# Kernel optimization log

Measured on AMD Instinct MI355X. Metric: run time of the kernel, lower is better.

Reference implementation:

```python
import jax, jax.numpy as jnp
import numpy as np

K = 3  # reassembly kernel size (hardcoded in module)
S = 2  # upsample scale (hardcoded)
PAD = K // 2


def _nearest_up2(t):
    # F.interpolate(scale_factor=2, mode='nearest') on NCHW
    return jnp.repeat(jnp.repeat(t, 2, axis=2), 2, axis=3)


def _patches3x3(t):
    # F.unfold(kernel=3, pad=1) -> [B, C, 9, H, W], k = ki*3 + kj (row-major)
    B, C, H, W = t.shape
    tp = jnp.pad(t, ((0, 0), (0, 0), (PAD, PAD), (PAD, PAD)))
    return jnp.stack([tp[:, :, i:i + H, j:j + W] for i in range(K) for j in range(K)], axis=2)


def setup_inputs() -> dict:
    key = jax.random.key(0)
    k1, k2 = jax.random.split(key)
    x = jax.random.normal(k1, (2, 256, 128, 128), dtype=jnp.float32)
    W_off = jax.random.normal(k2, (2, 1, 5, 5), dtype=jnp.float32) * 1e-3  # normal_init std=0.001
    b_off = jnp.zeros((2,), dtype=jnp.float32)
    return {"x": x, "W_off": W_off, "b_off": b_off}


def reference(x, W_off, b_off):
    B, C, H, W = x.shape
    H2, W2 = S * H, S * W

    mean = jnp.mean(x, axis=1, keepdims=True)  # [B,1,H,W]

    # offset = tanh(conv5x5(nearest_up2(mean))) / 4 -> [B,2,2H,2W]
    mean_up = _nearest_up2(mean)
    off = jax.lax.conv_general_dilated(mean_up, W_off, (1, 1), ((2, 2), (2, 2)))
    offset = jnp.tanh(off + b_off[None, :, None, None]) / 4.0

    # center buffer: pixel_shuffle of [1,8,1,1]; per 2x2 cell, channel 0 varies with j, channel 1 with i
    cell = jnp.array([[[-0.25, 0.25], [-0.25, 0.25]],
                      [[-0.25, -0.25], [0.25, 0.25]]], dtype=x.dtype)  # [2(ch),2(i),2(j)]
    center = jnp.broadcast_to(cell[:, None, :, None, :], (2, H, 2, W, 2)).reshape(2, H2, W2)

    shift = center[None] + offset  # [B,2,2H,2W]

    # neighbor grid: n0 (fast, width) = [-1,0,1]*3 ; n1 (slow, height) = repeat([-1,0,1],3)
    n0 = jnp.tile(jnp.array([-1.0, 0.0, 1.0], dtype=x.dtype), 3)        # [9]
    n1 = jnp.repeat(jnp.array([-1.0, 0.0, 1.0], dtype=x.dtype), 3)      # [9]
    d2 = (shift[:, 0:1] - n0[None, :, None, None]) ** 2 + \
         (shift[:, 1:2] - n1[None, :, None, None]) ** 2                 # [B,9,2H,2W]
    kernels = 1.0 / (d2 + 0.2)

    # grad gating from 3x3 neighborhood of mean
    pm = _patches3x3(mean)[:, 0]            # [B,9,H,W]
    grad = pm - mean                        # broadcast over k
    grad = 1.0 / (grad ** 2 + 1.0)
    logits = _nearest_up2(grad) * kernels   # [B,9,2H,2W]
    kernels = jax.nn.softmax(logits, axis=1)

    # CARAFE: out[b,c,2h+p,2w+q] = sum_k kernels[b,k,2h+p,2w+q] * patches[b,c,k,h,w]
    patches = _patches3x3(x)                        # [B,C,9,H,W]
    Kr = kernels.reshape(B, K * K, H, S, W, S)      # [B,9,H,2,W,2]
    out = jnp.einsum('bkhpwq,bckhw->bchpwq', Kr, patches).reshape(B, C, H2, W2)
    return out
```

## Files before the change

kernel.cpp:

```cpp
#include <hip/hip_runtime.h>
#include <math.h>

#define B 2
#define C 256
#define H 128
#define W 128
#define H2 256
#define W2 256
#define CPT 16
#define TW 16

typedef float vfloat4 __attribute__((ext_vector_type(4)));

__device__ __forceinline__ float frcp(float x) { return __builtin_amdgcn_rcpf(x); }
__device__ __forceinline__ float fast_tanh(float x) {
    float e = __expf(2.0f * x);
    return 1.0f - 2.0f * frcp(e + 1.0f);
}

__device__ __forceinline__ void nt_store4(float* p, const float4& v) {
    vfloat4 t; t.x = v.x; t.y = v.y; t.z = v.z; t.w = v.w;
    __builtin_nontemporal_store(t, (vfloat4*)p);
}

__global__ __launch_bounds__(1024) void mean_kernel(const float* __restrict__ x,
                                                    float* __restrict__ mean) {
    int bh = blockIdx.x;
    int b = bh / H, h = bh % H;
    int tid = threadIdx.x;
    int g  = tid >> 5;
    int w4 = tid & 31;

    const float4* xb = (const float4*)x + (size_t)b * C * (H * W / 4)
                       + (size_t)h * (W / 4) + w4;
    const size_t cstride = H * W / 4;

    float4 acc = make_float4(0.f, 0.f, 0.f, 0.f);
    #pragma unroll
    for (int i = 0; i < C / 32; ++i) {
        float4 v = xb[(size_t)(g * (C / 32) + i) * cstride];
        acc.x += v.x; acc.y += v.y; acc.z += v.z; acc.w += v.w;
    }

    __shared__ float4 sm[1024];
    sm[tid] = acc;
    __syncthreads();
    for (int s = 16; s >= 1; s >>= 1) {
        if (g < s) {
            float4 o = sm[tid + s * 32];
            acc.x += o.x; acc.y += o.y; acc.z += o.z; acc.w += o.w;
            sm[tid] = acc;
        }
        __syncthreads();
    }
    if (g == 0) {
        const float inv = 1.0f / C;
        float4 m = make_float4(acc.x * inv, acc.y * inv, acc.z * inv, acc.w * inv);
        ((float4*)mean)[(size_t)bh * (W / 4) + w4] = m;
    }
}

__global__ __launch_bounds__(256) void weights_kernel(const float* __restrict__ mean,
                                                      const float* __restrict__ Woff,
                                                      const float* __restrict__ boff,
                                                      float* __restrict__ Kw) {
    __shared__ float sm[10][12];
    __shared__ float sW[50];
    __shared__ float sb[2];

    int b  = blockIdx.z;
    int x0 = blockIdx.x * TW;
    int y0 = blockIdx.y * TW;
    int h0 = y0 >> 1, w0 = x0 >> 1;
    int tid = threadIdx.x;

    if (tid < 100) {
        int lh = tid / 10, lw = tid % 10;
        int hh = h0 - 1 + lh, ww = w0 - 1 + lw;
        sm[lh][lw] = (hh >= 0 && hh < H && ww >= 0 && ww < W)
                         ? mean[(size_t)b * H * W + hh * W + ww] : 0.f;
    }
    if (tid >= 128 && tid < 178) sW[tid - 128] = Woff[tid - 128];
    if (tid >= 192 && tid < 194) sb[tid - 192] = boff[tid - 192];
    __syncthreads();

    int tx = tid & 15, ty = tid >> 4;
    int y = y0 + ty, x = x0 + tx;

    float off0 = 0.f, off1 = 0.f;
    #pragma unroll
    for (int u = 0; u < 5; ++u) {
        int lh = ((y + u - 2) >> 1) - (h0 - 1);
        #pragma unroll
        for (int v = 0; v < 5; ++v) {
            int lw = ((x + v - 2) >> 1) - (w0 - 1);
            float m = sm[lh][lw];
            off0 += m * sW[u * 5 + v];
            off1 += m * sW[25 + u * 5 + v];
        }
    }
    float s0 = fast_tanh(off0 + sb[0]) * 0.25f + ((x & 1) ? 0.25f : -0.25f);
    float s1 = fast_tanh(off1 + sb[1]) * 0.25f + ((y & 1) ? 0.25f : -0.25f);

    int lhc = (ty >> 1) + 1;
    int lwc = (tx >> 1) + 1;
    float mc = sm[lhc][lwc];

    float lg[9];
    float mx = -1e30f;
    #pragma unroll
    for (int k = 0; k < 9; ++k) {
        int di = k / 3 - 1, dj = k % 3 - 1;
        float pm = sm[lhc + di][lwc + dj];
        float g = pm - mc;
        float grad = frcp(g * g + 1.0f);
        float d0 = s0 - (float)dj;
        float d1 = s1 - (float)di;
        float kern = frcp(d0 * d0 + d1 * d1 + 0.2f);
        float l = grad * kern;
        lg[k] = l;
        mx = fmaxf(mx, l);
    }
    float sum = 0.f;
    #pragma unroll
    for (int k = 0; k < 9; ++k) { lg[k] = __expf(lg[k] - mx); sum += lg[k]; }
    float inv = frcp(sum);

    float* o = Kw + (size_t)b * 9 * (H2 * W2) + (size_t)y * W2 + x;
    #pragma unroll
    for (int k = 0; k < 9; ++k) o[(size_t)k * (H2 * W2)] = lg[k] * inv;
}

__global__ __launch_bounds__(256) void carafe_kernel(const float* __restrict__ x,
                                                     const float* __restrict__ Kw,
                                                     float* __restrict__ out) {
    int idx = blockIdx.x * blockDim.x + threadIdx.x;
    int w2 = idx & 63;
    int h  = (idx >> 6) & (H - 1);
    int cg = (idx >> 13) & (C / CPT - 1);
    int b  = idx >> 17;

    int x0 = 4 * w2;
    int y0 = 2 * h;

    const float* kb = Kw + (size_t)b * 9 * (H2 * W2) + (size_t)y0 * W2 + x0;
    float4 wk[2][9];
    #pragma unroll
    for (int k = 0; k < 9; ++k) {
        wk[0][k] = *(const float4*)(kb + (size_t)k * (H2 * W2));
        wk[1][k] = *(const float4*)(kb + (size_t)k * (H2 * W2) + W2);
    }

    float rm0 = (h == 0)     ? 0.f : 1.f;
    float rm2 = (h == H - 1) ? 0.f : 1.f;
    float cl  = (w2 == 0)    ? 0.f : 1.f;
    float cr  = (w2 == 63)   ? 0.f : 1.f;
    #pragma unroll
    for (int pp = 0; pp < 2; ++pp)
        #pragma unroll
        for (int k = 0; k < 9; ++k) {
            int ki = k / 3, kj = k % 3;
            float r  = (ki == 0) ? rm0 : ((ki == 2) ? rm2 : 1.f);
            float ma = (kj == 0) ? r * cl : r;
            float mb = (kj == 2) ? r * cr : r;
            wk[pp][k].x *= ma; wk[pp][k].y *= ma;
            wk[pp][k].z *= mb; wk[pp][k].w *= mb;
        }

    int r0 = (h == 0) ? 0 : h - 1;
    int r2 = (h == H - 1) ? H - 1 : h + 1;

    const float* xc = x + (size_t)(b * C + cg * CPT) * (H * W);
    const float2* row0 = (const float2*)(xc + (size_t)r0 * W) + w2;
    const float2* row1 = (const float2*)(xc + (size_t)h  * W) + w2;
    const float2* row2 = (const float2*)(xc + (size_t)r2 * W) + w2;

    float* ob = out + (size_t)(b * C + cg * CPT) * (H2 * W2)
                    + (size_t)y0 * W2 + x0;

    #pragma unroll 2
    for (int cc = 0; cc < CPT; ++cc) {
        float2 v0 = row0[0];
        float2 v1 = row1[0];
        float2 v2 = row2[0];

        float e[3][4];
        e[0][1] = v0.x; e[0][2] = v0.y;
        e[1][1] = v1.x; e[1][2] = v1.y;
        e[2][1] = v2.x; e[2][2] = v2.y;
        e[0][0] = __shfl_up(v0.y, 1);   e[0][3] = __shfl_down(v0.x, 1);
        e[1][0] = __shfl_up(v1.y, 1);   e[1][3] = __shfl_down(v1.x, 1);
        e[2][0] = __shfl_up(v2.y, 1);   e[2][3] = __shfl_down(v2.x, 1);

        float4 a0 = make_float4(0.f, 0.f, 0.f, 0.f);
        float4 a1 = make_float4(0.f, 0.f, 0.f, 0.f);
        #pragma unroll
        for (int k = 0; k < 9; ++k) {
            int ki = k / 3, kj = k % 3;
            float pa = e[ki][kj];
            float pb = e[ki][kj + 1];
            a0.x += wk[0][k].x * pa; a0.y += wk[0][k].y * pa;
            a0.z += wk[0][k].z * pb; a0.w += wk[0][k].w * pb;
            a1.x += wk[1][k].x * pa; a1.y += wk[1][k].y * pa;
            a1.z += wk[1][k].z * pb; a1.w += wk[1][k].w * pb;
        }
        nt_store4(ob, a0);
        nt_store4(ob + W2, a1);

        row0 = (const float2*)((const float*)row0 + H * W);
        row1 = (const float2*)((const float*)row1 + H * W);
        row2 = (const float2*)((const float*)row2 + H * W);
        ob += (size_t)H2 * W2;
    }
}

extern "C" void kernel_launch(void* const* d_in, const int* in_sizes, int n_in,
                              void* d_out, int out_size, void* d_ws, size_t ws_size,
                              hipStream_t stream) {
    const float* x    = (const float*)d_in[0];
    const float* Woff = (const float*)d_in[1];
    const float* boff = (const float*)d_in[2];
    float* out = (float*)d_out;

    float* mean = (float*)d_ws;
    float* Kw   = mean + (size_t)B * H * W;

    mean_kernel<<<B * H, 1024, 0, stream>>>(x, mean);

    dim3 wgrid(W2 / TW, H2 / TW, B);
    weights_kernel<<<wgrid, 256, 0, stream>>>(mean, Woff, boff, Kw);

    int mt = B * (C / CPT) * H * (W / 2);
    carafe_kernel<<<mt / 256, 256, 0, stream>>>(x, Kw, out);
}
```

Baseline: 173.7 us.

## Fuse reassembly-weight computation into CARAFE kernel and drop weight buffer

The separate weights kernel and the 9-plane weight buffer in global memory are removed. Each CARAFE thread now loads its 3x3 neighbourhood of the channel mean, shares edges with its lane neighbours via shuffles, and computes the offset conv, tanh, gating and softmax for its 2x4 output pixels in registers. This removes one launch and the write and re-read of the weight planes. In exchange the weight math is recomputed once per channel group (16 times), which raises ALU work and register pressure. The softmax also drops the max subtraction, relying on the logits being bounded.

```diff
diff --git a/kernel.cpp b/kernel.cpp
--- a/kernel.cpp
+++ b/kernel.cpp
@@ -8,7 +8,6 @@
 #define H2 256
 #define W2 256
 #define CPT 16
-#define TW 16
 
 typedef float vfloat4 __attribute__((ext_vector_type(4)));
 
@@ -17,7 +16,6 @@
     float e = __expf(2.0f * x);
     return 1.0f - 2.0f * frcp(e + 1.0f);
 }
-
 __device__ __forceinline__ void nt_store4(float* p, const float4& v) {
     vfloat4 t; t.x = v.x; t.y = v.y; t.z = v.z; t.w = v.w;
     __builtin_nontemporal_store(t, (vfloat4*)p);
@@ -60,115 +58,97 @@
     }
 }
 
-__global__ __launch_bounds__(256) void weights_kernel(const float* __restrict__ mean,
-                                                      const float* __restrict__ Woff,
-                                                      const float* __restrict__ boff,
-                                                      float* __restrict__ Kw) {
-    __shared__ float sm[10][12];
+__global__ __launch_bounds__(256) void carafe_fused(const float* __restrict__ x,
+                                                    const float* __restrict__ mean,
+                                                    const float* __restrict__ Woff,
+                                                    const float* __restrict__ boff,
+                                                    float* __restrict__ out) {
     __shared__ float sW[50];
     __shared__ float sb[2];
-
-    int b  = blockIdx.z;
-    int x0 = blockIdx.x * TW;
-    int y0 = blockIdx.y * TW;
-    int h0 = y0 >> 1, w0 = x0 >> 1;
     int tid = threadIdx.x;
-
-    if (tid < 100) {
-        int lh = tid / 10, lw = tid % 10;
-        int hh = h0 - 1 + lh, ww = w0 - 1 + lw;
-        sm[lh][lw] = (hh >= 0 && hh < H && ww >= 0 && ww < W)
-                         ? mean[(size_t)b * H * W + hh * W + ww] : 0.f;
-    }
-    if (tid >= 128 && tid < 178) sW[tid - 128] = Woff[tid - 128];
-    if (tid >= 192 && tid < 194) sb[tid - 192] = boff[tid - 192];
+    if (tid < 50) sW[tid] = Woff[tid];
+    else if (tid < 52) sb[tid - 50] = boff[tid - 50];
     __syncthreads();
 
-    int tx = tid & 15, ty = tid >> 4;
-    int y = y0 + ty, x = x0 + tx;
-
-    float off0 = 0.f, off1 = 0.f;
-    #pragma unroll
-    for (int u = 0; u < 5; ++u) {
-        int lh = ((y + u - 2) >> 1) - (h0 - 1);
-        #pragma unroll
-        for (int v = 0; v < 5; ++v) {
-            int lw = ((x + v - 2) >> 1) - (w0 - 1);
-            float m = sm[lh][lw];
-            off0 += m * sW[u * 5 + v];
-            off1 += m * sW[25 + u * 5 + v];
-        }
-    }
-    float s0 = fast_tanh(off0 + sb[0]) * 0.25f + ((x & 1) ? 0.25f : -0.25f);
-    float s1 = fast_tanh(off1 + sb[1]) * 0.25f + ((y & 1) ? 0.25f : -0.25f);
-
-    int lhc = (ty >> 1) + 1;
-    int lwc = (tx >> 1) + 1;
-    float mc = sm[lhc][lwc];
-
-    float lg[9];
-    float mx = -1e30f;
-    #pragma unroll
-    for (int k = 0; k < 9; ++k) {
-        int di = k / 3 - 1, dj = k % 3 - 1;
-        float pm = sm[lhc + di][lwc + dj];
-        float g = pm - mc;
-        float grad = frcp(g * g + 1.0f);
-        float d0 = s0 - (float)dj;
-        float d1 = s1 - (float)di;
-        float kern = frcp(d0 * d0 + d1 * d1 + 0.2f);
-        float l = grad * kern;
-        lg[k] = l;
-        mx = fmaxf(mx, l);
-    }
-    float sum = 0.f;
-    #pragma unroll
-    for (int k = 0; k < 9; ++k) { lg[k] = __expf(lg[k] - mx); sum += lg[k]; }
-    float inv = frcp(sum);
-
-    float* o = Kw + (size_t)b * 9 * (H2 * W2) + (size_t)y * W2 + x;
-    #pragma unroll
-    for (int k = 0; k < 9; ++k) o[(size_t)k * (H2 * W2)] = lg[k] * inv;
-}
-
-__global__ __launch_bounds__(256) void carafe_kernel(const float* __restrict__ x,
-                                                     const float* __restrict__ Kw,
-                                                     float* __restrict__ out) {
-    int idx = blockIdx.x * blockDim.x + threadIdx.x;
+    int idx = blockIdx.x * blockDim.x + tid;
     int w2 = idx & 63;
     int h  = (idx >> 6) & (H - 1);
     int cg = (idx >> 13) & (C / CPT - 1);
     int b  = idx >> 17;
 
-    int x0 = 4 * w2;
-    int y0 = 2 * h;
-
-    const float* kb = Kw + (size_t)b * 9 * (H2 * W2) + (size_t)y0 * W2 + x0;
-    float4 wk[2][9];
-    #pragma unroll
-    for (int k = 0; k < 9; ++k) {
-        wk[0][k] = *(const float4*)(kb + (size_t)k * (H2 * W2));
-        wk[1][k] = *(const float4*)(kb + (size_t)k * (H2 * W2) + W2);
-    }
-
-    float rm0 = (h == 0)     ? 0.f : 1.f;
-    float rm2 = (h == H - 1) ? 0.f : 1.f;
-    float cl  = (w2 == 0)    ? 0.f : 1.f;
-    float cr  = (w2 == 63)   ? 0.f : 1.f;
-    #pragma unroll
-    for (int pp = 0; pp < 2; ++pp)
-        #pragma unroll
-        for (int k = 0; k < 9; ++k) {
-            int ki = k / 3, kj = k % 3;
-            float r  = (ki == 0) ? rm0 : ((ki == 2) ? rm2 : 1.f);
-            float ma = (kj == 0) ? r * cl : r;
-            float mb = (kj == 2) ? r * cr : r;
-            wk[pp][k].x *= ma; wk[pp][k].y *= ma;
-            wk[pp][k].z *= mb; wk[pp][k].w *= mb;
-        }
-
     int r0 = (h == 0) ? 0 : h - 1;
     int r2 = (h == H - 1) ? H - 1 : h + 1;
+    float rm0 = (h == 0)      ? 0.f : 1.f;
+    float rm2 = (h == H - 1)  ? 0.f : 1.f;
+    float cl  = (w2 == 0)     ? 0.f : 1.f;
+    float cr  = (w2 == 63)    ? 0.f : 1.f;
+
+    const float* mb = mean + (size_t)b * H * W;
+    float2 u0 = ((const float2*)(mb + (size_t)r0 * W))[w2];
+    float2 u1 = ((const float2*)(mb + (size_t)h  * W))[w2];
+    float2 u2 = ((const float2*)(mb + (size_t)r2 * W))[w2];
+
+    float m[3][4];
+    m[0][1] = u0.x; m[0][2] = u0.y;
+    m[1][1] = u1.x; m[1][2] = u1.y;
+    m[2][1] = u2.x; m[2][2] = u2.y;
+    m[0][0] = __shfl_up(u0.y, 1);  m[0][3] = __shfl_down(u0.x, 1);
+    m[1][0] = __shfl_up(u1.y, 1);  m[1][3] = __shfl_down(u1.x, 1);
+    m[2][0] = __shfl_up(u2.y, 1);  m[2][3] = __shfl_down(u2.x, 1);
+    #pragma unroll
+    for (int c = 0; c < 4; ++c) { m[0][c] *= rm0; m[2][c] *= rm2; }
+    #pragma unroll
+    for (int r = 0; r < 3; ++r) { m[r][0] *= cl; m[r][3] *= cr; }
+
+    float wgt[2][9][4];
+    #pragma unroll
+    for (int pp = 0; pp < 2; ++pp) {
+        #pragma unroll
+        for (int j = 0; j < 4; ++j) {
+            float off0 = 0.f, off1 = 0.f;
+            #pragma unroll
+            for (int u = 0; u < 5; ++u) {
+                const int rr = ((pp + u - 2) >> 1) + 1;
+                #pragma unroll
+                for (int v = 0; v < 5; ++v) {
+                    const int cc = ((j + v - 2) >> 1) + 1;
+                    float mm = m[rr][cc];
+                    off0 += mm * sW[u * 5 + v];
+                    off1 += mm * sW[25 + u * 5 + v];
+                }
+            }
+            float s0 = fast_tanh(off0 + sb[0]) * 0.25f + ((j & 1) ? 0.25f : -0.25f);
+            float s1 = fast_tanh(off1 + sb[1]) * 0.25f + (pp ? 0.25f : -0.25f);
+
+            const int jc = 1 + (j >> 1);
+            float mc = m[1][jc];
+
+            float lg[9];
+            float sum = 0.f;
+            #pragma unroll
+            for (int k = 0; k < 9; ++k) {
+                const int di = k / 3 - 1, dj = k % 3 - 1;
+                float pm = m[1 + di][jc + dj];
+                float g = pm - mc;
+                float grad = frcp(g * g + 1.0f);
+                float d0 = s0 - (float)dj;
+                float d1 = s1 - (float)di;
+                float kern = frcp(d0 * d0 + d1 * d1 + 0.2f);
+                lg[k] = __expf(grad * kern);
+                sum += lg[k];
+            }
+            float inv = frcp(sum);
+            #pragma unroll
+            for (int k = 0; k < 9; ++k) {
+                const int ki = k / 3, kj = k % 3;
+                float r   = (ki == 0) ? rm0 : ((ki == 2) ? rm2 : 1.f);
+                float msk = (kj == 0) ? ((j < 2)  ? r * cl : r)
+                          : (kj == 2) ? ((j >= 2) ? r * cr : r)
+                                      : r;
+                wgt[pp][k][j] = lg[k] * inv * msk;
+            }
+        }
+    }
 
     const float* xc = x + (size_t)(b * C + cg * CPT) * (H * W);
     const float2* row0 = (const float2*)(xc + (size_t)r0 * W) + w2;
@@ -176,10 +156,10 @@
     const float2* row2 = (const float2*)(xc + (size_t)r2 * W) + w2;
 
     float* ob = out + (size_t)(b * C + cg * CPT) * (H2 * W2)
-                    + (size_t)y0 * W2 + x0;
+                    + (size_t)(2 * h) * W2 + 4 * w2;
 
     #pragma unroll 2
-    for (int cc = 0; cc < CPT; ++cc) {
+    for (int cc2 = 0; cc2 < CPT; ++cc2) {
         float2 v0 = row0[0];
         float2 v1 = row1[0];
         float2 v2 = row2[0];
@@ -196,13 +176,13 @@
         float4 a1 = make_float4(0.f, 0.f, 0.f, 0.f);
         #pragma unroll
         for (int k = 0; k < 9; ++k) {
-            int ki = k / 3, kj = k % 3;
+            const int ki = k / 3, kj = k % 3;
             float pa = e[ki][kj];
             float pb = e[ki][kj + 1];
-            a0.x += wk[0][k].x * pa; a0.y += wk[0][k].y * pa;
-            a0.z += wk[0][k].z * pb; a0.w += wk[0][k].w * pb;
-            a1.x += wk[1][k].x * pa; a1.y += wk[1][k].y * pa;
-            a1.z += wk[1][k].z * pb; a1.w += wk[1][k].w * pb;
+            a0.x += wgt[0][k][0] * pa;  a0.y += wgt[0][k][1] * pa;
+            a0.z += wgt[0][k][2] * pb;  a0.w += wgt[0][k][3] * pb;
+            a1.x += wgt[1][k][0] * pa;  a1.y += wgt[1][k][1] * pa;
+            a1.z += wgt[1][k][2] * pb;  a1.w += wgt[1][k][3] * pb;
         }
         nt_store4(ob, a0);
         nt_store4(ob + W2, a1);
@@ -223,13 +203,9 @@
     float* out = (float*)d_out;
 
     float* mean = (float*)d_ws;
-    float* Kw   = mean + (size_t)B * H * W;
 
     mean_kernel<<<B * H, 1024, 0, stream>>>(x, mean);
 
-    dim3 wgrid(W2 / TW, H2 / TW, B);
-    weights_kernel<<<wgrid, 256, 0, stream>>>(mean, Woff, boff, Kw);
-
     int mt = B * (C / CPT) * H * (W / 2);
-    carafe_kernel<<<mt / 256, 256, 0, stream>>>(x, Kw, out);
-}
+    carafe_fused<<<mt / 256, 256, 0, stream>>>(x, mean, Woff, boff, out);
+}
```

After: 173.2 us. Within noise of the previous version (-0.3%).
